# Kernel optimization log

Hardware: AMD Instinct MI355X
Metric: run time of the kernel (lower is better)

## Reference

```python
import jax, jax.numpy as jnp
import numpy as np

N_NODES = 50000
N_EDGES = 640000
IN_CH = 128
OUT_CH = 128
HID = 2 * OUT_CH  # 256


def _glorot(key, shape):
    fan_in, fan_out = shape
    lim = np.sqrt(6.0 / (fan_in + fan_out)).astype(np.float32)
    return jax.random.uniform(key, shape, jnp.float32, -lim, lim)


def setup_inputs() -> dict:
    key = jax.random.key(0)
    ks = jax.random.split(key, 8)
    x = jax.random.normal(ks[0], (N_NODES, IN_CH), jnp.float32)
    edge_index = jax.random.randint(ks[1], (2, N_EDGES), 0, N_NODES, jnp.int64)
    # SAGEConv layer 1: lin_l (neighbor branch, with bias), lin_r (root branch, no bias)
    w1_l = _glorot(ks[2], (IN_CH, HID))
    b1_l = jnp.zeros((HID,), jnp.float32)
    w1_r = _glorot(ks[3], (IN_CH, HID))
    # SAGEConv layer 2
    w2_l = _glorot(ks[4], (HID, OUT_CH))
    b2_l = jnp.zeros((OUT_CH,), jnp.float32)
    w2_r = _glorot(ks[5], (HID, OUT_CH))
    return {"x": x, "edge_index": edge_index,
            "w1_l": w1_l, "b1_l": b1_l, "w1_r": w1_r,
            "w2_l": w2_l, "b2_l": b2_l, "w2_r": w2_r}


def _sage_conv(x, src, dst, w_l, b_l, w_r):
    # mean aggregation of source-node features onto destination nodes
    msgs = x[src]                                       # [E, C] gather
    agg = jax.ops.segment_sum(msgs, dst, num_segments=N_NODES)  # [N, C]
    cnt = jax.ops.segment_sum(jnp.ones((src.shape[0],), x.dtype), dst,
                              num_segments=N_NODES)     # [N]
    mean = agg / jnp.maximum(cnt, 1.0)[:, None]
    # out = lin_l(mean_neighbors) + lin_r(x_root)
    return mean @ w_l + b_l + x @ w_r


def reference(x, edge_index, w1_l, b1_l, w1_r, w2_l, b2_l, w2_r):
    src, dst = edge_index[0], edge_index[1]
    h = _sage_conv(x, src, dst, w1_l, b1_l, w1_r)
    h = jax.nn.relu(h)
    return _sage_conv(h, src, dst, w2_l, b2_l, w2_r)
```

## Files before the change

### kernel.cpp

```cpp
#include <hip/hip_runtime.h>

#define N_NODES 50000
#define N_EDGES 640000
#define IN_CH 128
#define OUT_CH 128
#define HID 256
#define M_PAD 50048
#define CAP 64

typedef unsigned int uint;
typedef unsigned short ushort;

__device__ __forceinline__ ushort f2b(float f) {
    uint u = __float_as_uint(f);
    u += 0x7FFFu + ((u >> 16) & 1u);
    return (ushort)(u >> 16);
}
__device__ __forceinline__ float b2f_lo(uint u) { return __uint_as_float(u << 16); }
__device__ __forceinline__ float b2f_hi(uint u) { return __uint_as_float(u & 0xFFFF0000u); }
__device__ __forceinline__ uint packb(float lo, float hi) {
    return (uint)f2b(lo) | ((uint)f2b(hi) << 16);
}

__device__ __forceinline__ void gload_lds16(const ushort* g, ushort* l) {
    __builtin_amdgcn_global_load_lds(
        (const __attribute__((address_space(1))) void*)g,
        (__attribute__((address_space(3))) void*)l, 16, 0, 0);
}

__global__ __launch_bounds__(256) void prep(
    const int* __restrict__ src, const int* __restrict__ dst,
    const float* __restrict__ x, const float* __restrict__ w1l,
    const float* __restrict__ w1r, const float* __restrict__ w2l,
    const float* __restrict__ w2r, int* __restrict__ cnt,
    int* __restrict__ col, ushort* __restrict__ xcat,
    ushort* __restrict__ w1f, ushort* __restrict__ w2f) {
    int b = blockIdx.x;
    if (b < 2500) {
        int e = b * 256 + threadIdx.x;
        int d = dst[e];
        int p = atomicAdd(&cnt[d], 1);
        if (p < CAP) col[d * CAP + p] = src[e];
    } else {
        int id = (b - 2500) * 256 + threadIdx.x;
        if (id < 800000) {
            long long base = (long long)id * 8;
            float4 a = *(const float4*)(x + base);
            float4 c = *(const float4*)(x + base + 4);
            uint4 o;
            o.x = packb(a.x, a.y);
            o.y = packb(a.z, a.w);
            o.z = packb(c.x, c.y);
            o.w = packb(c.z, c.w);
            int row = id >> 4;
            int cc = id & 15;
            ((uint4*)xcat)[(size_t)row * 32 + 16 + cc] = o;
        } else if (id < 865536) {
            int i = id - 800000;
            int n0 = i >> 12, kk = (i >> 9) & 7, lane = (i >> 3) & 63, j = i & 7;
            int n = n0 * 16 + (lane & 15);
            int k = kk * 32 + (lane >> 4) * 8 + j;
            float v = (k < 128) ? w1l[k * 256 + n] : w1r[(k - 128) * 256 + n];
            w1f[i] = f2b(v);
        } else {
            int i = id - 865536;
            int n0 = i >> 12, kk = (i >> 9) & 7, lane = (i >> 3) & 63, j = i & 7;
            int n = n0 * 16 + (lane & 15);
            int k = kk * 32 + (lane >> 4) * 8 + j;
            float v = (n < 128) ? w2l[k * 128 + n] : w2r[k * 128 + (n - 128)];
            w2f[i] = f2b(v);
        }
    }
}

__global__ __launch_bounds__(256) void aggregate_mean1(
    const int* __restrict__ cnt, const int* __restrict__ col,
    ushort* __restrict__ xcat) {
    int t = blockIdx.x * 256 + threadIdx.x;
    int node = t >> 4;
    int q = t & 15;
    if (node >= N_NODES) return;
    int degf = cnt[node];
    int deg = min(degf, CAP);
    const int* cb = col + node * CAP;
    float acc[8] = {0.f, 0.f, 0.f, 0.f, 0.f, 0.f, 0.f, 0.f};
    const uint4* f4 = (const uint4*)xcat;
    int j = 0;
    for (; j + 4 <= deg; j += 4) {
        int4 s4 = *(const int4*)(cb + j);
        uint4 v0 = f4[(size_t)s4.x * 32 + 16 + q];
        uint4 v1 = f4[(size_t)s4.y * 32 + 16 + q];
        uint4 v2 = f4[(size_t)s4.z * 32 + 16 + q];
        uint4 v3 = f4[(size_t)s4.w * 32 + 16 + q];
        acc[0] += b2f_lo(v0.x) + b2f_lo(v1.x) + b2f_lo(v2.x) + b2f_lo(v3.x);
        acc[1] += b2f_hi(v0.x) + b2f_hi(v1.x) + b2f_hi(v2.x) + b2f_hi(v3.x);
        acc[2] += b2f_lo(v0.y) + b2f_lo(v1.y) + b2f_lo(v2.y) + b2f_lo(v3.y);
        acc[3] += b2f_hi(v0.y) + b2f_hi(v1.y) + b2f_hi(v2.y) + b2f_hi(v3.y);
        acc[4] += b2f_lo(v0.z) + b2f_lo(v1.z) + b2f_lo(v2.z) + b2f_lo(v3.z);
        acc[5] += b2f_hi(v0.z) + b2f_hi(v1.z) + b2f_hi(v2.z) + b2f_hi(v3.z);
        acc[6] += b2f_lo(v0.w) + b2f_lo(v1.w) + b2f_lo(v2.w) + b2f_lo(v3.w);
        acc[7] += b2f_hi(v0.w) + b2f_hi(v1.w) + b2f_hi(v2.w) + b2f_hi(v3.w);
    }
    for (; j < deg; ++j) {
        uint4 v = f4[(size_t)cb[j] * 32 + 16 + q];
        acc[0] += b2f_lo(v.x); acc[1] += b2f_hi(v.x);
        acc[2] += b2f_lo(v.y); acc[3] += b2f_hi(v.y);
        acc[4] += b2f_lo(v.z); acc[5] += b2f_hi(v.z);
        acc[6] += b2f_lo(v.w); acc[7] += b2f_hi(v.w);
    }
    float inv = 1.0f / fmaxf((float)degf, 1.0f);
    uint4 o;
    o.x = packb(acc[0] * inv, acc[1] * inv);
    o.y = packb(acc[2] * inv, acc[3] * inv);
    o.z = packb(acc[4] * inv, acc[5] * inv);
    o.w = packb(acc[6] * inv, acc[7] * inv);
    ((uint4*)xcat)[(size_t)node * 32 + q] = o;
}

__global__ __launch_bounds__(256) void combine2(
    const ushort* __restrict__ hw, const int* __restrict__ cnt,
    const int* __restrict__ col, const float* __restrict__ bias,
    float* __restrict__ out) {
    int t = blockIdx.x * 256 + threadIdx.x;
    int node = t >> 4;
    int q = t & 15;
    if (node >= N_NODES) return;
    int degf = cnt[node];
    int deg = min(degf, CAP);
    const int* cb = col + node * CAP;
    float acc[8] = {0.f, 0.f, 0.f, 0.f, 0.f, 0.f, 0.f, 0.f};
    const uint4* f4 = (const uint4*)hw;
    int j = 0;
    for (; j + 4 <= deg; j += 4) {
        int4 s4 = *(const int4*)(cb + j);
        uint4 v0 = f4[(size_t)s4.x * 32 + q];
        uint4 v1 = f4[(size_t)s4.y * 32 + q];
        uint4 v2 = f4[(size_t)s4.z * 32 + q];
        uint4 v3 = f4[(size_t)s4.w * 32 + q];
        acc[0] += b2f_lo(v0.x) + b2f_lo(v1.x) + b2f_lo(v2.x) + b2f_lo(v3.x);
        acc[1] += b2f_hi(v0.x) + b2f_hi(v1.x) + b2f_hi(v2.x) + b2f_hi(v3.x);
        acc[2] += b2f_lo(v0.y) + b2f_lo(v1.y) + b2f_lo(v2.y) + b2f_lo(v3.y);
        acc[3] += b2f_hi(v0.y) + b2f_hi(v1.y) + b2f_hi(v2.y) + b2f_hi(v3.y);
        acc[4] += b2f_lo(v0.z) + b2f_lo(v1.z) + b2f_lo(v2.z) + b2f_lo(v3.z);
        acc[5] += b2f_hi(v0.z) + b2f_hi(v1.z) + b2f_hi(v2.z) + b2f_hi(v3.z);
        acc[6] += b2f_lo(v0.w) + b2f_lo(v1.w) + b2f_lo(v2.w) + b2f_lo(v3.w);
        acc[7] += b2f_hi(v0.w) + b2f_hi(v1.w) + b2f_hi(v2.w) + b2f_hi(v3.w);
    }
    for (; j < deg; ++j) {
        uint4 v = f4[(size_t)cb[j] * 32 + q];
        acc[0] += b2f_lo(v.x); acc[1] += b2f_hi(v.x);
        acc[2] += b2f_lo(v.y); acc[3] += b2f_hi(v.y);
        acc[4] += b2f_lo(v.z); acc[5] += b2f_hi(v.z);
        acc[6] += b2f_lo(v.w); acc[7] += b2f_hi(v.w);
    }
    float inv = 1.0f / fmaxf((float)degf, 1.0f);
    uint4 r = f4[(size_t)node * 32 + 16 + q];
    float4 b0 = *(const float4*)(bias + q * 8);
    float4 b1 = *(const float4*)(bias + q * 8 + 4);
    float4 o0, o1;
    o0.x = acc[0] * inv + b2f_lo(r.x) + b0.x;
    o0.y = acc[1] * inv + b2f_hi(r.x) + b0.y;
    o0.z = acc[2] * inv + b2f_lo(r.y) + b0.z;
    o0.w = acc[3] * inv + b2f_hi(r.y) + b0.w;
    o1.x = acc[4] * inv + b2f_lo(r.z) + b1.x;
    o1.y = acc[5] * inv + b2f_hi(r.z) + b1.y;
    o1.z = acc[6] * inv + b2f_lo(r.w) + b1.z;
    o1.w = acc[7] * inv + b2f_hi(r.w) + b1.w;
    *(float4*)(out + (size_t)node * 128 + q * 8) = o0;
    *(float4*)(out + (size_t)node * 128 + q * 8 + 4) = o1;
}

using bf16x8 = __attribute__((ext_vector_type(8))) short;
using f32x4  = __attribute__((ext_vector_type(4))) float;

__global__ __launch_bounds__(256) void fused_gemm(
    const ushort* __restrict__ A, const ushort* __restrict__ w1f,
    const ushort* __restrict__ w2f, const float* __restrict__ b1,
    ushort* __restrict__ hw) {
    __shared__ alignas(16) ushort tile[32 * 256];

    const int tid = threadIdx.x;
    const int lane = tid & 63;
    const int wave = tid >> 6;
    const int quad = lane >> 4;
    const int l16 = lane & 15;
    const int bm = blockIdx.x * 32;

#pragma unroll
    for (int r = 0; r < 4; ++r) {
        int row = r * 8 + (tid >> 5);
        int c = tid & 31;
        int src = (c & 24) | ((c & 7) ^ (row & 7));
        gload_lds16(A + (size_t)(bm + row) * 256 + src * 8, &tile[row * 256 + c * 8]);
    }

    f32x4 acc[2][4];
#pragma unroll
    for (int rt = 0; rt < 2; ++rt)
#pragma unroll
        for (int ct = 0; ct < 4; ++ct) acc[rt][ct] = (f32x4){0.f, 0.f, 0.f, 0.f};

    const size_t bstep = 64 * 8;
    const ushort* w1b = w1f + (((size_t)(wave * 4) * 8) * 64 + lane) * 8;
    const ushort* w2b = w2f + (((size_t)(wave * 4) * 8) * 64 + lane) * 8;

    bf16x8 bc[4], bn[4];
#pragma unroll
    for (int ct = 0; ct < 4; ++ct)
        bc[ct] = *(const bf16x8*)(w1b + (size_t)ct * 8 * bstep);

    __syncthreads();

#pragma unroll
    for (int kk = 0; kk < 8; ++kk) {
        if (kk < 7) {
#pragma unroll
            for (int ct = 0; ct < 4; ++ct)
                bn[ct] = *(const bf16x8*)(w1b + ((size_t)ct * 8 + kk + 1) * bstep);
        }
        bf16x8 af[2];
#pragma unroll
        for (int rt = 0; rt < 2; ++rt) {
            int row = rt * 16 + l16;
            int c = kk * 4 + quad;
            int slot = (c & 24) | ((c & 7) ^ (row & 7));
            af[rt] = *(const bf16x8*)&tile[row * 256 + slot * 8];
        }
#pragma unroll
        for (int ct = 0; ct < 4; ++ct) {
#pragma unroll
            for (int rt = 0; rt < 2; ++rt)
                acc[rt][ct] = __builtin_amdgcn_mfma_f32_16x16x32_bf16(
                    af[rt], bc[ct], acc[rt][ct], 0, 0, 0);
        }
#pragma unroll
        for (int ct = 0; ct < 4; ++ct) bc[ct] = bn[ct];
    }
    __syncthreads();

#pragma unroll
    for (int ct = 0; ct < 4; ++ct) {
        int colg = wave * 64 + ct * 16 + l16;
        float bv = b1[colg];
        int cc = colg >> 3;
        int off = colg & 7;
#pragma unroll
        for (int rt = 0; rt < 2; ++rt) {
#pragma unroll
            for (int reg = 0; reg < 4; ++reg) {
                int row = rt * 16 + quad * 4 + reg;
                int slot = (cc & 24) | ((cc & 7) ^ (row & 7));
                tile[row * 256 + slot * 8 + off] = f2b(fmaxf(acc[rt][ct][reg] + bv, 0.0f));
            }
        }
    }

#pragma unroll
    for (int rt = 0; rt < 2; ++rt)
#pragma unroll
        for (int ct = 0; ct < 4; ++ct) acc[rt][ct] = (f32x4){0.f, 0.f, 0.f, 0.f};

#pragma unroll
    for (int ct = 0; ct < 4; ++ct)
        bc[ct] = *(const bf16x8*)(w2b + (size_t)ct * 8 * bstep);

    __syncthreads();

#pragma unroll
    for (int kk = 0; kk < 8; ++kk) {
        if (kk < 7) {
#pragma unroll
            for (int ct = 0; ct < 4; ++ct)
                bn[ct] = *(const bf16x8*)(w2b + ((size_t)ct * 8 + kk + 1) * bstep);
        }
        bf16x8 af[2];
#pragma unroll
        for (int rt = 0; rt < 2; ++rt) {
            int row = rt * 16 + l16;
            int c = kk * 4 + quad;
            int slot = (c & 24) | ((c & 7) ^ (row & 7));
            af[rt] = *(const bf16x8*)&tile[row * 256 + slot * 8];
        }
#pragma unroll
        for (int ct = 0; ct < 4; ++ct) {
#pragma unroll
            for (int rt = 0; rt < 2; ++rt)
                acc[rt][ct] = __builtin_amdgcn_mfma_f32_16x16x32_bf16(
                    af[rt], bc[ct], acc[rt][ct], 0, 0, 0);
        }
#pragma unroll
        for (int ct = 0; ct < 4; ++ct) bc[ct] = bn[ct];
    }
    __syncthreads();

#pragma unroll
    for (int ct = 0; ct < 4; ++ct) {
        int colg = wave * 64 + ct * 16 + l16;
        int cc = colg >> 3;
        int off = colg & 7;
#pragma unroll
        for (int rt = 0; rt < 2; ++rt) {
#pragma unroll
            for (int reg = 0; reg < 4; ++reg) {
                int row = rt * 16 + quad * 4 + reg;
                int slot = (cc & 24) | ((cc & 7) ^ (row & 7));
                tile[row * 256 + slot * 8 + off] = f2b(acc[rt][ct][reg]);
            }
        }
    }
    __syncthreads();
#pragma unroll
    for (int r = 0; r < 4; ++r) {
        int row = r * 8 + (tid >> 5);
        int c = tid & 31;
        int slot = (c & 24) | ((c & 7) ^ (row & 7));
        uint4 v = *(const uint4*)&tile[row * 256 + slot * 8];
        *(uint4*)(hw + (size_t)(bm + row) * 256 + c * 8) = v;
    }
}

extern "C" void kernel_launch(void* const* d_in, const int* in_sizes, int n_in,
                              void* d_out, int out_size, void* d_ws, size_t ws_size,
                              hipStream_t stream) {
    const float* x    = (const float*)d_in[0];
    const int*   ei   = (const int*)d_in[1];
    const float* w1_l = (const float*)d_in[2];
    const float* b1_l = (const float*)d_in[3];
    const float* w1_r = (const float*)d_in[4];
    const float* w2_l = (const float*)d_in[5];
    const float* b2_l = (const float*)d_in[6];
    const float* w2_r = (const float*)d_in[7];
    float* out = (float*)d_out;

    const int* src = ei;
    const int* dst = ei + N_EDGES;

    int* cnt = (int*)d_ws;
    int* col = cnt + N_NODES;
    size_t int_bytes = (size_t)(N_NODES + N_NODES * CAP) * 4;
    size_t ofs = (int_bytes + 15) & ~(size_t)15;
    ushort* xcat = (ushort*)((char*)d_ws + ofs);
    ushort* hw   = xcat + (size_t)M_PAD * HID;
    ushort* w1f  = hw + (size_t)M_PAD * HID;
    ushort* w2f  = w1f + HID * HID;

    hipMemsetAsync(cnt, 0, (size_t)N_NODES * sizeof(int), stream);

    prep<<<6137, 256, 0, stream>>>(src, dst, x, w1_l, w1_r, w2_l, w2_r,
                                   cnt, col, xcat, w1f, w2f);

    aggregate_mean1<<<N_NODES * 16 / 256, 256, 0, stream>>>(cnt, col, xcat);
    fused_gemm<<<M_PAD / 32, 256, 0, stream>>>(xcat, w1f, w2f, b1_l, hw);
    combine2<<<N_NODES * 16 / 256, 256, 0, stream>>>(hw, cnt, col, b2_l, out);
}
```

Measured before the change: 230.2 us.

## Fuse layer-1 mean aggregation into the fused GEMM kernel's LDS tile load

Removes the separate aggregate_mean1 kernel. Each fused_gemm block now gathers and averages neighbor features for its 32 rows and writes the bf16 mean straight into a swizzled LDS tile, while the root half is loaded asynchronously. The shared tile is split into left and right halves. This saves one launch and the global write and re-read of the aggregated half of xcat. In exchange, the GEMM blocks now stall on irregular gathers before their MFMA work, and each thread handles 16 channels with only 2-edge unrolling, so there is less memory-level parallelism than before.

Measured after the change: 226.7 us, median of 2. About the same (-1.5%).

```diff
diff --git a/kernel.cpp b/kernel.cpp
--- a/kernel.cpp
+++ b/kernel.cpp
@@ -73,50 +73,6 @@
     }
 }
 
-__global__ __launch_bounds__(256) void aggregate_mean1(
-    const int* __restrict__ cnt, const int* __restrict__ col,
-    ushort* __restrict__ xcat) {
-    int t = blockIdx.x * 256 + threadIdx.x;
-    int node = t >> 4;
-    int q = t & 15;
-    if (node >= N_NODES) return;
-    int degf = cnt[node];
-    int deg = min(degf, CAP);
-    const int* cb = col + node * CAP;
-    float acc[8] = {0.f, 0.f, 0.f, 0.f, 0.f, 0.f, 0.f, 0.f};
-    const uint4* f4 = (const uint4*)xcat;
-    int j = 0;
-    for (; j + 4 <= deg; j += 4) {
-        int4 s4 = *(const int4*)(cb + j);
-        uint4 v0 = f4[(size_t)s4.x * 32 + 16 + q];
-        uint4 v1 = f4[(size_t)s4.y * 32 + 16 + q];
-        uint4 v2 = f4[(size_t)s4.z * 32 + 16 + q];
-        uint4 v3 = f4[(size_t)s4.w * 32 + 16 + q];
-        acc[0] += b2f_lo(v0.x) + b2f_lo(v1.x) + b2f_lo(v2.x) + b2f_lo(v3.x);
-        acc[1] += b2f_hi(v0.x) + b2f_hi(v1.x) + b2f_hi(v2.x) + b2f_hi(v3.x);
-        acc[2] += b2f_lo(v0.y) + b2f_lo(v1.y) + b2f_lo(v2.y) + b2f_lo(v3.y);
-        acc[3] += b2f_hi(v0.y) + b2f_hi(v1.y) + b2f_hi(v2.y) + b2f_hi(v3.y);
-        acc[4] += b2f_lo(v0.z) + b2f_lo(v1.z) + b2f_lo(v2.z) + b2f_lo(v3.z);
-        acc[5] += b2f_hi(v0.z) + b2f_hi(v1.z) + b2f_hi(v2.z) + b2f_hi(v3.z);
-        acc[6] += b2f_lo(v0.w) + b2f_lo(v1.w) + b2f_lo(v2.w) + b2f_lo(v3.w);
-        acc[7] += b2f_hi(v0.w) + b2f_hi(v1.w) + b2f_hi(v2.w) + b2f_hi(v3.w);
-    }
-    for (; j < deg; ++j) {
-        uint4 v = f4[(size_t)cb[j] * 32 + 16 + q];
-        acc[0] += b2f_lo(v.x); acc[1] += b2f_hi(v.x);
-        acc[2] += b2f_lo(v.y); acc[3] += b2f_hi(v.y);
-        acc[4] += b2f_lo(v.z); acc[5] += b2f_hi(v.z);
-        acc[6] += b2f_lo(v.w); acc[7] += b2f_hi(v.w);
-    }
-    float inv = 1.0f / fmaxf((float)degf, 1.0f);
-    uint4 o;
-    o.x = packb(acc[0] * inv, acc[1] * inv);
-    o.y = packb(acc[2] * inv, acc[3] * inv);
-    o.z = packb(acc[4] * inv, acc[5] * inv);
-    o.w = packb(acc[6] * inv, acc[7] * inv);
-    ((uint4*)xcat)[(size_t)node * 32 + q] = o;
-}
-
 __global__ __launch_bounds__(256) void combine2(
     const ushort* __restrict__ hw, const int* __restrict__ cnt,
     const int* __restrict__ col, const float* __restrict__ bias,
@@ -174,10 +130,12 @@
 using f32x4  = __attribute__((ext_vector_type(4))) float;
 
 __global__ __launch_bounds__(256) void fused_gemm(
-    const ushort* __restrict__ A, const ushort* __restrict__ w1f,
+    const ushort* __restrict__ A, const int* __restrict__ cnt,
+    const int* __restrict__ col, const ushort* __restrict__ w1f,
     const ushort* __restrict__ w2f, const float* __restrict__ b1,
     ushort* __restrict__ hw) {
-    __shared__ alignas(16) ushort tile[32 * 256];
+    __shared__ alignas(16) ushort tileL[32 * 128];
+    __shared__ alignas(16) ushort tileR[32 * 128];
 
     const int tid = threadIdx.x;
     const int lane = tid & 63;
@@ -187,27 +145,92 @@
     const int bm = blockIdx.x * 32;
 
 #pragma unroll
-    for (int r = 0; r < 4; ++r) {
-        int row = r * 8 + (tid >> 5);
-        int c = tid & 31;
-        int src = (c & 24) | ((c & 7) ^ (row & 7));
-        gload_lds16(A + (size_t)(bm + row) * 256 + src * 8, &tile[row * 256 + c * 8]);
-    }
-
-    f32x4 acc[2][4];
-#pragma unroll
-    for (int rt = 0; rt < 2; ++rt)
-#pragma unroll
-        for (int ct = 0; ct < 4; ++ct) acc[rt][ct] = (f32x4){0.f, 0.f, 0.f, 0.f};
+    for (int r = 0; r < 2; ++r) {
+        int row = r * 16 + (tid >> 4);
+        int kc = tid & 15;
+        int src = 16 + ((kc & 8) | ((kc & 7) ^ (row & 7)));
+        gload_lds16(A + (size_t)(bm + row) * 256 + src * 8,
+                    &tileR[row * 128 + kc * 8]);
+    }
 
     const size_t bstep = 64 * 8;
     const ushort* w1b = w1f + (((size_t)(wave * 4) * 8) * 64 + lane) * 8;
     const ushort* w2b = w2f + (((size_t)(wave * 4) * 8) * 64 + lane) * 8;
-
     bf16x8 bc[4], bn[4];
 #pragma unroll
     for (int ct = 0; ct < 4; ++ct)
         bc[ct] = *(const bf16x8*)(w1b + (size_t)ct * 8 * bstep);
+
+    {
+        int rw = tid >> 3;
+        int q8 = tid & 7;
+        int node = bm + rw;
+        int degf = 0, deg = 0;
+        if (node < N_NODES) { degf = cnt[node]; deg = min(degf, CAP); }
+        const int* cb = col + (size_t)node * CAP;
+        const uint4* f4 = (const uint4*)A;
+        float acc[16];
+#pragma unroll
+        for (int i = 0; i < 16; ++i) acc[i] = 0.f;
+        int j = 0;
+        for (; j + 2 <= deg; j += 2) {
+            int2 s2 = *(const int2*)(cb + j);
+            uint4 a0 = f4[(size_t)s2.x * 32 + 16 + q8 * 2];
+            uint4 a1 = f4[(size_t)s2.x * 32 + 17 + q8 * 2];
+            uint4 c0 = f4[(size_t)s2.y * 32 + 16 + q8 * 2];
+            uint4 c1 = f4[(size_t)s2.y * 32 + 17 + q8 * 2];
+            acc[0] += b2f_lo(a0.x) + b2f_lo(c0.x);
+            acc[1] += b2f_hi(a0.x) + b2f_hi(c0.x);
+            acc[2] += b2f_lo(a0.y) + b2f_lo(c0.y);
+            acc[3] += b2f_hi(a0.y) + b2f_hi(c0.y);
+            acc[4] += b2f_lo(a0.z) + b2f_lo(c0.z);
+            acc[5] += b2f_hi(a0.z) + b2f_hi(c0.z);
+            acc[6] += b2f_lo(a0.w) + b2f_lo(c0.w);
+            acc[7] += b2f_hi(a0.w) + b2f_hi(c0.w);
+            acc[8]  += b2f_lo(a1.x) + b2f_lo(c1.x);
+            acc[9]  += b2f_hi(a1.x) + b2f_hi(c1.x);
+            acc[10] += b2f_lo(a1.y) + b2f_lo(c1.y);
+            acc[11] += b2f_hi(a1.y) + b2f_hi(c1.y);
+            acc[12] += b2f_lo(a1.z) + b2f_lo(c1.z);
+            acc[13] += b2f_hi(a1.z) + b2f_hi(c1.z);
+            acc[14] += b2f_lo(a1.w) + b2f_lo(c1.w);
+            acc[15] += b2f_hi(a1.w) + b2f_hi(c1.w);
+        }
+        if (j < deg) {
+            int s = cb[j];
+            uint4 a0 = f4[(size_t)s * 32 + 16 + q8 * 2];
+            uint4 a1 = f4[(size_t)s * 32 + 17 + q8 * 2];
+            acc[0] += b2f_lo(a0.x);  acc[1] += b2f_hi(a0.x);
+            acc[2] += b2f_lo(a0.y);  acc[3] += b2f_hi(a0.y);
+            acc[4] += b2f_lo(a0.z);  acc[5] += b2f_hi(a0.z);
+            acc[6] += b2f_lo(a0.w);  acc[7] += b2f_hi(a0.w);
+            acc[8]  += b2f_lo(a1.x); acc[9]  += b2f_hi(a1.x);
+            acc[10] += b2f_lo(a1.y); acc[11] += b2f_hi(a1.y);
+            acc[12] += b2f_lo(a1.z); acc[13] += b2f_hi(a1.z);
+            acc[14] += b2f_lo(a1.w); acc[15] += b2f_hi(a1.w);
+        }
+        float inv = 1.0f / fmaxf((float)degf, 1.0f);
+        int kc0 = q8 * 2, kc1 = q8 * 2 + 1;
+        int s0 = (kc0 & 8) | ((kc0 & 7) ^ (rw & 7));
+        int s1 = (kc1 & 8) | ((kc1 & 7) ^ (rw & 7));
+        uint4 o0, o1;
+        o0.x = packb(acc[0] * inv, acc[1] * inv);
+        o0.y = packb(acc[2] * inv, acc[3] * inv);
+        o0.z = packb(acc[4] * inv, acc[5] * inv);
+        o0.w = packb(acc[6] * inv, acc[7] * inv);
+        o1.x = packb(acc[8] * inv, acc[9] * inv);
+        o1.y = packb(acc[10] * inv, acc[11] * inv);
+        o1.z = packb(acc[12] * inv, acc[13] * inv);
+        o1.w = packb(acc[14] * inv, acc[15] * inv);
+        *(uint4*)&tileL[rw * 128 + s0 * 8] = o0;
+        *(uint4*)&tileL[rw * 128 + s1 * 8] = o1;
+    }
+
+    f32x4 acc[2][4];
+#pragma unroll
+    for (int rt = 0; rt < 2; ++rt)
+#pragma unroll
+        for (int ct = 0; ct < 4; ++ct) acc[rt][ct] = (f32x4){0.f, 0.f, 0.f, 0.f};
 
     __syncthreads();
 
@@ -223,8 +246,10 @@
         for (int rt = 0; rt < 2; ++rt) {
             int row = rt * 16 + l16;
             int c = kk * 4 + quad;
-            int slot = (c & 24) | ((c & 7) ^ (row & 7));
-            af[rt] = *(const bf16x8*)&tile[row * 256 + slot * 8];
+            int hc = c & 15;
+            int slot = (hc & 8) | ((hc & 7) ^ (row & 7));
+            const ushort* base = (c < 16) ? tileL : tileR;
+            af[rt] = *(const bf16x8*)&base[row * 128 + slot * 8];
         }
 #pragma unroll
         for (int ct = 0; ct < 4; ++ct) {
@@ -243,14 +268,16 @@
         int colg = wave * 64 + ct * 16 + l16;
         float bv = b1[colg];
         int cc = colg >> 3;
+        int hc = cc & 15;
         int off = colg & 7;
+        ushort* base = (cc < 16) ? tileL : tileR;
 #pragma unroll
         for (int rt = 0; rt < 2; ++rt) {
 #pragma unroll
             for (int reg = 0; reg < 4; ++reg) {
                 int row = rt * 16 + quad * 4 + reg;
-                int slot = (cc & 24) | ((cc & 7) ^ (row & 7));
-                tile[row * 256 + slot * 8 + off] = f2b(fmaxf(acc[rt][ct][reg] + bv, 0.0f));
+                int slot = (hc & 8) | ((hc & 7) ^ (row & 7));
+                base[row * 128 + slot * 8 + off] = f2b(fmaxf(acc[rt][ct][reg] + bv, 0.0f));
             }
         }
     }
@@ -278,8 +305,10 @@
         for (int rt = 0; rt < 2; ++rt) {
             int row = rt * 16 + l16;
             int c = kk * 4 + quad;
-            int slot = (c & 24) | ((c & 7) ^ (row & 7));
-            af[rt] = *(const bf16x8*)&tile[row * 256 + slot * 8];
+            int hc = c & 15;
+            int slot = (hc & 8) | ((hc & 7) ^ (row & 7));
+            const ushort* base = (c < 16) ? tileL : tileR;
+            af[rt] = *(const bf16x8*)&base[row * 128 + slot * 8];
         }
 #pragma unroll
         for (int ct = 0; ct < 4; ++ct) {
@@ -297,14 +326,16 @@
     for (int ct = 0; ct < 4; ++ct) {
         int colg = wave * 64 + ct * 16 + l16;
         int cc = colg >> 3;
+        int hc = cc & 15;
         int off = colg & 7;
+        ushort* base = (cc < 16) ? tileL : tileR;
 #pragma unroll
         for (int rt = 0; rt < 2; ++rt) {
 #pragma unroll
             for (int reg = 0; reg < 4; ++reg) {
                 int row = rt * 16 + quad * 4 + reg;
-                int slot = (cc & 24) | ((cc & 7) ^ (row & 7));
-                tile[row * 256 + slot * 8 + off] = f2b(acc[rt][ct][reg]);
+                int slot = (hc & 8) | ((hc & 7) ^ (row & 7));
+                base[row * 128 + slot * 8 + off] = f2b(acc[rt][ct][reg]);
             }
         }
     }
@@ -313,8 +344,10 @@
     for (int r = 0; r < 4; ++r) {
         int row = r * 8 + (tid >> 5);
         int c = tid & 31;
-        int slot = (c & 24) | ((c & 7) ^ (row & 7));
-        uint4 v = *(const uint4*)&tile[row * 256 + slot * 8];
+        int hc = c & 15;
+        int slot = (hc & 8) | ((hc & 7) ^ (row & 7));
+        const ushort* base = (c < 16) ? tileL : tileR;
+        uint4 v = *(const uint4*)&base[row * 128 + slot * 8];
         *(uint4*)(hw + (size_t)(bm + row) * 256 + c * 8) = v;
     }
 }
@@ -346,10 +379,9 @@
 
     hipMemsetAsync(cnt, 0, (size_t)N_NODES * sizeof(int), stream);
 
-    prep<<<6137, 256, 0, stream>>>(src, dst, x, w1_l, w1_r, w2_l, w2_r,
-                                   cnt, col, xcat, w1f, w2f);
-
-    aggregate_mean1<<<N_NODES * 16 / 256, 256, 0, stream>>>(cnt, col, xcat);
-    fused_gemm<<<M_PAD / 32, 256, 0, stream>>>(xcat, w1f, w2f, b1_l, hw);
+    prep<<<2500 + 3637, 256, 0, stream>>>(src, dst, x, w1_l, w1_r, w2_l, w2_r,
+                                          cnt, col, xcat, w1f, w2f);
+
+    fused_gemm<<<M_PAD / 32, 256, 0, stream>>>(xcat, cnt, col, w1f, w2f, b1_l, hw);
     combine2<<<N_NODES * 16 / 256, 256, 0, stream>>>(hw, cnt, col, b2_l, out);
 }
```

## Split gather tables into channel slices for cache-friendly neighbor aggregation

Applied to the files above, without the earlier changes.

Stores the bf16 node features and the GEMM output in a sliced layout, where each 16-channel slice is contiguous across all nodes. Aggregation and combine kernels now assign each block one slice and 128 nodes, so concurrently running blocks gather from a much smaller working set that fits in L2/LLC. This costs an extra write of x in the slice layout during prep and more scattered row stores from the GEMM epilogue, and each gather is now only 32 bytes per node per slice instead of one full row.

Result: slower. 243.1 us (+5.6%).

```diff
diff --git a/kernel.cpp b/kernel.cpp
--- a/kernel.cpp
+++ b/kernel.cpp
@@ -34,7 +34,8 @@
     const float* __restrict__ w1r, const float* __restrict__ w2l,
     const float* __restrict__ w2r, int* __restrict__ cnt,
     int* __restrict__ col, ushort* __restrict__ xcat,
-    ushort* __restrict__ w1f, ushort* __restrict__ w2f) {
+    ushort* __restrict__ xs, ushort* __restrict__ w1f,
+    ushort* __restrict__ w2f) {
     int b = blockIdx.x;
     if (b < 2500) {
         int e = b * 256 + threadIdx.x;
@@ -55,6 +56,7 @@
             int row = id >> 4;
             int cc = id & 15;
             ((uint4*)xcat)[(size_t)row * 32 + 16 + cc] = o;
+            ((uint4*)xs)[(size_t)((cc >> 1) * M_PAD + row) * 2 + (cc & 1)] = o;
         } else if (id < 865536) {
             int i = id - 800000;
             int n0 = i >> 12, kk = (i >> 9) & 7, lane = (i >> 3) & 63, j = i & 7;
@@ -73,25 +75,27 @@
     }
 }
 
-__global__ __launch_bounds__(256) void aggregate_mean1(
+__global__ __launch_bounds__(256) void aggregate_s(
     const int* __restrict__ cnt, const int* __restrict__ col,
-    ushort* __restrict__ xcat) {
-    int t = blockIdx.x * 256 + threadIdx.x;
-    int node = t >> 4;
-    int q = t & 15;
+    const ushort* __restrict__ xs, ushort* __restrict__ xcat) {
+    int slice = blockIdx.x & 7;
+    int chunk = blockIdx.x >> 3;
+    int node = chunk * 128 + (threadIdx.x >> 1);
+    int half = threadIdx.x & 1;
     if (node >= N_NODES) return;
     int degf = cnt[node];
     int deg = min(degf, CAP);
-    const int* cb = col + node * CAP;
+    const int* cb = col + (size_t)node * CAP;
+    const uint4* xv = (const uint4*)xs;
+    const size_t gb = (size_t)slice * M_PAD * 2 + half;
     float acc[8] = {0.f, 0.f, 0.f, 0.f, 0.f, 0.f, 0.f, 0.f};
-    const uint4* f4 = (const uint4*)xcat;
     int j = 0;
     for (; j + 4 <= deg; j += 4) {
         int4 s4 = *(const int4*)(cb + j);
-        uint4 v0 = f4[(size_t)s4.x * 32 + 16 + q];
-        uint4 v1 = f4[(size_t)s4.y * 32 + 16 + q];
-        uint4 v2 = f4[(size_t)s4.z * 32 + 16 + q];
-        uint4 v3 = f4[(size_t)s4.w * 32 + 16 + q];
+        uint4 v0 = xv[gb + (size_t)s4.x * 2];
+        uint4 v1 = xv[gb + (size_t)s4.y * 2];
+        uint4 v2 = xv[gb + (size_t)s4.z * 2];
+        uint4 v3 = xv[gb + (size_t)s4.w * 2];
         acc[0] += b2f_lo(v0.x) + b2f_lo(v1.x) + b2f_lo(v2.x) + b2f_lo(v3.x);
         acc[1] += b2f_hi(v0.x) + b2f_hi(v1.x) + b2f_hi(v2.x) + b2f_hi(v3.x);
         acc[2] += b2f_lo(v0.y) + b2f_lo(v1.y) + b2f_lo(v2.y) + b2f_lo(v3.y);
@@ -102,7 +106,7 @@
         acc[7] += b2f_hi(v0.w) + b2f_hi(v1.w) + b2f_hi(v2.w) + b2f_hi(v3.w);
     }
     for (; j < deg; ++j) {
-        uint4 v = f4[(size_t)cb[j] * 32 + 16 + q];
+        uint4 v = xv[gb + (size_t)cb[j] * 2];
         acc[0] += b2f_lo(v.x); acc[1] += b2f_hi(v.x);
         acc[2] += b2f_lo(v.y); acc[3] += b2f_hi(v.y);
         acc[4] += b2f_lo(v.z); acc[5] += b2f_hi(v.z);
@@ -114,29 +118,31 @@
     o.y = packb(acc[2] * inv, acc[3] * inv);
     o.z = packb(acc[4] * inv, acc[5] * inv);
     o.w = packb(acc[6] * inv, acc[7] * inv);
-    ((uint4*)xcat)[(size_t)node * 32 + q] = o;
-}
-
-__global__ __launch_bounds__(256) void combine2(
-    const ushort* __restrict__ hw, const int* __restrict__ cnt,
+    ((uint4*)xcat)[(size_t)node * 32 + slice * 2 + half] = o;
+}
+
+__global__ __launch_bounds__(256) void combine2_s(
+    const ushort* __restrict__ hws, const int* __restrict__ cnt,
     const int* __restrict__ col, const float* __restrict__ bias,
     float* __restrict__ out) {
-    int t = blockIdx.x * 256 + threadIdx.x;
-    int node = t >> 4;
-    int q = t & 15;
+    int slice = blockIdx.x & 7;
+    int chunk = blockIdx.x >> 3;
+    int node = chunk * 128 + (threadIdx.x >> 1);
+    int half = threadIdx.x & 1;
     if (node >= N_NODES) return;
     int degf = cnt[node];
     int deg = min(degf, CAP);
-    const int* cb = col + node * CAP;
+    const int* cb = col + (size_t)node * CAP;
+    const uint4* hv = (const uint4*)hws;
+    const size_t gb = (size_t)slice * M_PAD * 2 + half;
     float acc[8] = {0.f, 0.f, 0.f, 0.f, 0.f, 0.f, 0.f, 0.f};
-    const uint4* f4 = (const uint4*)hw;
     int j = 0;
     for (; j + 4 <= deg; j += 4) {
         int4 s4 = *(const int4*)(cb + j);
-        uint4 v0 = f4[(size_t)s4.x * 32 + q];
-        uint4 v1 = f4[(size_t)s4.y * 32 + q];
-        uint4 v2 = f4[(size_t)s4.z * 32 + q];
-        uint4 v3 = f4[(size_t)s4.w * 32 + q];
+        uint4 v0 = hv[gb + (size_t)s4.x * 2];
+        uint4 v1 = hv[gb + (size_t)s4.y * 2];
+        uint4 v2 = hv[gb + (size_t)s4.z * 2];
+        uint4 v3 = hv[gb + (size_t)s4.w * 2];
         acc[0] += b2f_lo(v0.x) + b2f_lo(v1.x) + b2f_lo(v2.x) + b2f_lo(v3.x);
         acc[1] += b2f_hi(v0.x) + b2f_hi(v1.x) + b2f_hi(v2.x) + b2f_hi(v3.x);
         acc[2] += b2f_lo(v0.y) + b2f_lo(v1.y) + b2f_lo(v2.y) + b2f_lo(v3.y);
@@ -147,16 +153,17 @@
         acc[7] += b2f_hi(v0.w) + b2f_hi(v1.w) + b2f_hi(v2.w) + b2f_hi(v3.w);
     }
     for (; j < deg; ++j) {
-        uint4 v = f4[(size_t)cb[j] * 32 + q];
+        uint4 v = hv[gb + (size_t)cb[j] * 2];
         acc[0] += b2f_lo(v.x); acc[1] += b2f_hi(v.x);
         acc[2] += b2f_lo(v.y); acc[3] += b2f_hi(v.y);
         acc[4] += b2f_lo(v.z); acc[5] += b2f_hi(v.z);
         acc[6] += b2f_lo(v.w); acc[7] += b2f_hi(v.w);
     }
     float inv = 1.0f / fmaxf((float)degf, 1.0f);
-    uint4 r = f4[(size_t)node * 32 + 16 + q];
-    float4 b0 = *(const float4*)(bias + q * 8);
-    float4 b1 = *(const float4*)(bias + q * 8 + 4);
+    uint4 r = hv[(size_t)((8 + slice) * M_PAD + node) * 2 + half];
+    int c0 = slice * 16 + half * 8;
+    float4 b0 = *(const float4*)(bias + c0);
+    float4 b1 = *(const float4*)(bias + c0 + 4);
     float4 o0, o1;
     o0.x = acc[0] * inv + b2f_lo(r.x) + b0.x;
     o0.y = acc[1] * inv + b2f_hi(r.x) + b0.y;
@@ -166,8 +173,8 @@
     o1.y = acc[5] * inv + b2f_hi(r.z) + b1.y;
     o1.z = acc[6] * inv + b2f_lo(r.w) + b1.z;
     o1.w = acc[7] * inv + b2f_hi(r.w) + b1.w;
-    *(float4*)(out + (size_t)node * 128 + q * 8) = o0;
-    *(float4*)(out + (size_t)node * 128 + q * 8 + 4) = o1;
+    *(float4*)(out + (size_t)node * 128 + c0) = o0;
+    *(float4*)(out + (size_t)node * 128 + c0 + 4) = o1;
 }
 
 using bf16x8 = __attribute__((ext_vector_type(8))) short;
@@ -176,7 +183,7 @@
 __global__ __launch_bounds__(256) void fused_gemm(
     const ushort* __restrict__ A, const ushort* __restrict__ w1f,
     const ushort* __restrict__ w2f, const float* __restrict__ b1,
-    ushort* __restrict__ hw) {
+    ushort* __restrict__ hws) {
     __shared__ alignas(16) ushort tile[32 * 256];
 
     const int tid = threadIdx.x;
@@ -310,12 +317,14 @@
     }
     __syncthreads();
 #pragma unroll
-    for (int r = 0; r < 4; ++r) {
-        int row = r * 8 + (tid >> 5);
-        int c = tid & 31;
-        int slot = (c & 24) | ((c & 7) ^ (row & 7));
-        uint4 v = *(const uint4*)&tile[row * 256 + slot * 8];
-        *(uint4*)(hw + (size_t)(bm + row) * 256 + c * 8) = v;
+    for (int it = 0; it < 4; ++it) {
+        int sidx = it * 4 + wave;
+        int node = lane >> 1;
+        int hf = lane & 1;
+        int c = sidx * 2 + hf;
+        int slot = (c & 24) | ((c & 7) ^ (node & 7));
+        uint4 v = *(const uint4*)&tile[node * 256 + slot * 8];
+        ((uint4*)hws)[(size_t)(sidx * M_PAD + bm + node) * 2 + hf] = v;
     }
 }
 
@@ -340,16 +349,17 @@
     size_t int_bytes = (size_t)(N_NODES + N_NODES * CAP) * 4;
     size_t ofs = (int_bytes + 15) & ~(size_t)15;
     ushort* xcat = (ushort*)((char*)d_ws + ofs);
-    ushort* hw   = xcat + (size_t)M_PAD * HID;
-    ushort* w1f  = hw + (size_t)M_PAD * HID;
+    ushort* xs   = xcat + (size_t)M_PAD * HID;
+    ushort* hws  = xs + (size_t)8 * M_PAD * 16;
+    ushort* w1f  = hws + (size_t)16 * M_PAD * 16;
     ushort* w2f  = w1f + HID * HID;
 
     hipMemsetAsync(cnt, 0, (size_t)N_NODES * sizeof(int), stream);
 
-    prep<<<6137, 256, 0, stream>>>(src, dst, x, w1_l, w1_r, w2_l, w2_r,
-                                   cnt, col, xcat, w1f, w2f);
-
-    aggregate_mean1<<<N_NODES * 16 / 256, 256, 0, stream>>>(cnt, col, xcat);
-    fused_gemm<<<M_PAD / 32, 256, 0, stream>>>(xcat, w1f, w2f, b1_l, hw);
-    combine2<<<N_NODES * 16 / 256, 256, 0, stream>>>(hw, cnt, col, b2_l, out);
-}
+    prep<<<2500 + 3637, 256, 0, stream>>>(src, dst, x, w1_l, w1_r, w2_l, w2_r,
+                                          cnt, col, xcat, xs, w1f, w2f);
+
+    aggregate_s<<<8 * 391, 256, 0, stream>>>(cnt, col, xs, xcat);
+    fused_gemm<<<M_PAD / 32, 256, 0, stream>>>(xcat, w1f, w2f, b1_l, hws);
+    combine2_s<<<8 * 391, 256, 0, stream>>>(hws, cnt, col, b2_l, out);
+}
```

## Two-level bucketed CSR build and persistent double-buffered fused GEMM

Applied to the files above, without the earlier changes.

The edge-to-CSR construction changes from per-node global atomics to a two-stage scheme. Edges are first appended as (dst,src) pairs into 196 coarse bins of 256 nodes each, using padded bin counters. A new binplace kernel then scatters each bin into the per-node col lists using shared-memory atomics, which is meant to cut global atomic contention and the scattered writes. The fused GEMM becomes a persistent kernel with 512 blocks that loops over row tiles and prefetches the next A tile into a second LDS buffer while computing the current one. The costs are an extra kernel launch, an intermediate bin buffer, a hard BIN_CAP per bin, doubled LDS use and extra barriers per tile.

New measurement: 246.1 us. 6.9% more time.

```diff
diff --git a/kernel.cpp b/kernel.cpp
--- a/kernel.cpp
+++ b/kernel.cpp
@@ -7,6 +7,9 @@
 #define HID 256
 #define M_PAD 50048
 #define CAP 64
+#define BINS 196
+#define BIN_CAP 4096
+#define GEMM_GRID 512
 
 typedef unsigned int uint;
 typedef unsigned short ushort;
@@ -32,15 +35,17 @@
     const int* __restrict__ src, const int* __restrict__ dst,
     const float* __restrict__ x, const float* __restrict__ w1l,
     const float* __restrict__ w1r, const float* __restrict__ w2l,
-    const float* __restrict__ w2r, int* __restrict__ cnt,
-    int* __restrict__ col, ushort* __restrict__ xcat,
+    const float* __restrict__ w2r, int* __restrict__ bcnt,
+    int2* __restrict__ bins, ushort* __restrict__ xcat,
     ushort* __restrict__ w1f, ushort* __restrict__ w2f) {
     int b = blockIdx.x;
     if (b < 2500) {
         int e = b * 256 + threadIdx.x;
         int d = dst[e];
-        int p = atomicAdd(&cnt[d], 1);
-        if (p < CAP) col[d * CAP + p] = src[e];
+        int s = src[e];
+        int bb = d >> 8;
+        int p = atomicAdd(&bcnt[bb * 32], 1);
+        if (p < BIN_CAP) bins[(size_t)bb * BIN_CAP + p] = make_int2(d, s);
     } else {
         int id = (b - 2500) * 256 + threadIdx.x;
         if (id < 800000) {
@@ -73,6 +78,26 @@
     }
 }
 
+__global__ __launch_bounds__(256) void binplace(
+    const int* __restrict__ bcnt, const int2* __restrict__ bins,
+    int* __restrict__ cnt, int* __restrict__ col) {
+    __shared__ int lcnt[256];
+    int b = blockIdx.x;
+    lcnt[threadIdx.x] = 0;
+    __syncthreads();
+    int n = min(bcnt[b * 32], BIN_CAP);
+    int base = b << 8;
+    const int2* bb = bins + (size_t)b * BIN_CAP;
+    for (int i = threadIdx.x; i < n; i += 256) {
+        int2 e = bb[i];
+        int p = atomicAdd(&lcnt[e.x - base], 1);
+        if (p < CAP) col[(size_t)e.x * CAP + p] = e.y;
+    }
+    __syncthreads();
+    int node = base + threadIdx.x;
+    if (node < N_NODES) cnt[node] = lcnt[threadIdx.x];
+}
+
 __global__ __launch_bounds__(256) void aggregate_mean1(
     const int* __restrict__ cnt, const int* __restrict__ col,
     ushort* __restrict__ xcat) {
@@ -177,145 +202,169 @@
     const ushort* __restrict__ A, const ushort* __restrict__ w1f,
     const ushort* __restrict__ w2f, const float* __restrict__ b1,
     ushort* __restrict__ hw) {
-    __shared__ alignas(16) ushort tile[32 * 256];
+    __shared__ alignas(16) ushort buf[2][32 * 256];
 
     const int tid = threadIdx.x;
     const int lane = tid & 63;
     const int wave = tid >> 6;
     const int quad = lane >> 4;
     const int l16 = lane & 15;
-    const int bm = blockIdx.x * 32;
-
-#pragma unroll
-    for (int r = 0; r < 4; ++r) {
-        int row = r * 8 + (tid >> 5);
-        int c = tid & 31;
-        int src = (c & 24) | ((c & 7) ^ (row & 7));
-        gload_lds16(A + (size_t)(bm + row) * 256 + src * 8, &tile[row * 256 + c * 8]);
-    }
-
-    f32x4 acc[2][4];
-#pragma unroll
-    for (int rt = 0; rt < 2; ++rt)
-#pragma unroll
-        for (int ct = 0; ct < 4; ++ct) acc[rt][ct] = (f32x4){0.f, 0.f, 0.f, 0.f};
+    const int srow = tid >> 5;
+    const int sc = tid & 31;
+    const int NT = M_PAD / 32;
 
     const size_t bstep = 64 * 8;
     const ushort* w1b = w1f + (((size_t)(wave * 4) * 8) * 64 + lane) * 8;
     const ushort* w2b = w2f + (((size_t)(wave * 4) * 8) * 64 + lane) * 8;
 
-    bf16x8 bc[4], bn[4];
-#pragma unroll
-    for (int ct = 0; ct < 4; ++ct)
-        bc[ct] = *(const bf16x8*)(w1b + (size_t)ct * 8 * bstep);
-
+    {
+        int t = blockIdx.x;
+#pragma unroll
+        for (int r = 0; r < 4; ++r) {
+            int row = r * 8 + srow;
+            int sl = (sc & 24) | ((sc & 7) ^ (row & 7));
+            gload_lds16(A + (size_t)(t * 32 + row) * 256 + sl * 8,
+                        &buf[0][row * 256 + sc * 8]);
+        }
+    }
+    int cur = 0;
     __syncthreads();
 
-#pragma unroll
-    for (int kk = 0; kk < 8; ++kk) {
-        if (kk < 7) {
-#pragma unroll
-            for (int ct = 0; ct < 4; ++ct)
-                bn[ct] = *(const bf16x8*)(w1b + ((size_t)ct * 8 + kk + 1) * bstep);
-        }
-        bf16x8 af[2];
-#pragma unroll
-        for (int rt = 0; rt < 2; ++rt) {
-            int row = rt * 16 + l16;
-            int c = kk * 4 + quad;
-            int slot = (c & 24) | ((c & 7) ^ (row & 7));
-            af[rt] = *(const bf16x8*)&tile[row * 256 + slot * 8];
-        }
+    for (int t = blockIdx.x; t < NT; t += GEMM_GRID) {
+        ushort* tile = buf[cur];
+        const int bm = t * 32;
+
+        int tn = t + GEMM_GRID;
+        if (tn < NT) {
+            ushort* nb = buf[cur ^ 1];
+#pragma unroll
+            for (int r = 0; r < 4; ++r) {
+                int row = r * 8 + srow;
+                int sl = (sc & 24) | ((sc & 7) ^ (row & 7));
+                gload_lds16(A + (size_t)(tn * 32 + row) * 256 + sl * 8,
+                            &nb[row * 256 + sc * 8]);
+            }
+        }
+
+        f32x4 acc[2][4];
+#pragma unroll
+        for (int rt = 0; rt < 2; ++rt)
+#pragma unroll
+            for (int ct = 0; ct < 4; ++ct) acc[rt][ct] = (f32x4){0.f, 0.f, 0.f, 0.f};
+
+        bf16x8 bc[4], bn[4];
+#pragma unroll
+        for (int ct = 0; ct < 4; ++ct)
+            bc[ct] = *(const bf16x8*)(w1b + (size_t)ct * 8 * bstep);
+
+#pragma unroll
+        for (int kk = 0; kk < 8; ++kk) {
+            if (kk < 7) {
+#pragma unroll
+                for (int ct = 0; ct < 4; ++ct)
+                    bn[ct] = *(const bf16x8*)(w1b + ((size_t)ct * 8 + kk + 1) * bstep);
+            }
+            bf16x8 af[2];
+#pragma unroll
+            for (int rt = 0; rt < 2; ++rt) {
+                int row = rt * 16 + l16;
+                int c = kk * 4 + quad;
+                int slot = (c & 24) | ((c & 7) ^ (row & 7));
+                af[rt] = *(const bf16x8*)&tile[row * 256 + slot * 8];
+            }
+#pragma unroll
+            for (int ct = 0; ct < 4; ++ct) {
+#pragma unroll
+                for (int rt = 0; rt < 2; ++rt)
+                    acc[rt][ct] = __builtin_amdgcn_mfma_f32_16x16x32_bf16(
+                        af[rt], bc[ct], acc[rt][ct], 0, 0, 0);
+            }
+#pragma unroll
+            for (int ct = 0; ct < 4; ++ct) bc[ct] = bn[ct];
+        }
+        __syncthreads();
+
 #pragma unroll
         for (int ct = 0; ct < 4; ++ct) {
-#pragma unroll
-            for (int rt = 0; rt < 2; ++rt)
-                acc[rt][ct] = __builtin_amdgcn_mfma_f32_16x16x32_bf16(
-                    af[rt], bc[ct], acc[rt][ct], 0, 0, 0);
-        }
-#pragma unroll
-        for (int ct = 0; ct < 4; ++ct) bc[ct] = bn[ct];
-    }
-    __syncthreads();
-
-#pragma unroll
-    for (int ct = 0; ct < 4; ++ct) {
-        int colg = wave * 64 + ct * 16 + l16;
-        float bv = b1[colg];
-        int cc = colg >> 3;
-        int off = colg & 7;
-#pragma unroll
-        for (int rt = 0; rt < 2; ++rt) {
-#pragma unroll
-            for (int reg = 0; reg < 4; ++reg) {
-                int row = rt * 16 + quad * 4 + reg;
-                int slot = (cc & 24) | ((cc & 7) ^ (row & 7));
-                tile[row * 256 + slot * 8 + off] = f2b(fmaxf(acc[rt][ct][reg] + bv, 0.0f));
-            }
-        }
-    }
-
-#pragma unroll
-    for (int rt = 0; rt < 2; ++rt)
-#pragma unroll
-        for (int ct = 0; ct < 4; ++ct) acc[rt][ct] = (f32x4){0.f, 0.f, 0.f, 0.f};
-
-#pragma unroll
-    for (int ct = 0; ct < 4; ++ct)
-        bc[ct] = *(const bf16x8*)(w2b + (size_t)ct * 8 * bstep);
-
-    __syncthreads();
-
-#pragma unroll
-    for (int kk = 0; kk < 8; ++kk) {
-        if (kk < 7) {
-#pragma unroll
-            for (int ct = 0; ct < 4; ++ct)
-                bn[ct] = *(const bf16x8*)(w2b + ((size_t)ct * 8 + kk + 1) * bstep);
-        }
-        bf16x8 af[2];
-#pragma unroll
-        for (int rt = 0; rt < 2; ++rt) {
-            int row = rt * 16 + l16;
-            int c = kk * 4 + quad;
-            int slot = (c & 24) | ((c & 7) ^ (row & 7));
-            af[rt] = *(const bf16x8*)&tile[row * 256 + slot * 8];
-        }
+            int colg = wave * 64 + ct * 16 + l16;
+            float bv = b1[colg];
+            int cc = colg >> 3;
+            int off = colg & 7;
+#pragma unroll
+            for (int rt = 0; rt < 2; ++rt) {
+#pragma unroll
+                for (int reg = 0; reg < 4; ++reg) {
+                    int row = rt * 16 + quad * 4 + reg;
+                    int slot = (cc & 24) | ((cc & 7) ^ (row & 7));
+                    tile[row * 256 + slot * 8 + off] =
+                        f2b(fmaxf(acc[rt][ct][reg] + bv, 0.0f));
+                }
+            }
+        }
+
+#pragma unroll
+        for (int rt = 0; rt < 2; ++rt)
+#pragma unroll
+            for (int ct = 0; ct < 4; ++ct) acc[rt][ct] = (f32x4){0.f, 0.f, 0.f, 0.f};
+
+#pragma unroll
+        for (int ct = 0; ct < 4; ++ct)
+            bc[ct] = *(const bf16x8*)(w2b + (size_t)ct * 8 * bstep);
+
+        __syncthreads();
+
+#pragma unroll
+        for (int kk = 0; kk < 8; ++kk) {
+            if (kk < 7) {
+#pragma unroll
+                for (int ct = 0; ct < 4; ++ct)
+                    bn[ct] = *(const bf16x8*)(w2b + ((size_t)ct * 8 + kk + 1) * bstep);
+            }
+            bf16x8 af[2];
+#pragma unroll
+            for (int rt = 0; rt < 2; ++rt) {
+                int row = rt * 16 + l16;
+                int c = kk * 4 + quad;
+                int slot = (c & 24) | ((c & 7) ^ (row & 7));
+                af[rt] = *(const bf16x8*)&tile[row * 256 + slot * 8];
+            }
+#pragma unroll
+            for (int ct = 0; ct < 4; ++ct) {
+#pragma unroll
+                for (int rt = 0; rt < 2; ++rt)
+                    acc[rt][ct] = __builtin_amdgcn_mfma_f32_16x16x32_bf16(
+                        af[rt], bc[ct], acc[rt][ct], 0, 0, 0);
+            }
+#pragma unroll
+            for (int ct = 0; ct < 4; ++ct) bc[ct] = bn[ct];
+        }
+        __syncthreads();
+
 #pragma unroll
         for (int ct = 0; ct < 4; ++ct) {
-#pragma unroll
-            for (int rt = 0; rt < 2; ++rt)
-                acc[rt][ct] = __builtin_amdgcn_mfma_f32_16x16x32_bf16(
-                    af[rt], bc[ct], acc[rt][ct], 0, 0, 0);
-        }
-#pragma unroll
-        for (int ct = 0; ct < 4; ++ct) bc[ct] = bn[ct];
-    }
-    __syncthreads();
-
-#pragma unroll
-    for (int ct = 0; ct < 4; ++ct) {
-        int colg = wave * 64 + ct * 16 + l16;
-        int cc = colg >> 3;
-        int off = colg & 7;
-#pragma unroll
-        for (int rt = 0; rt < 2; ++rt) {
-#pragma unroll
-            for (int reg = 0; reg < 4; ++reg) {
-                int row = rt * 16 + quad * 4 + reg;
-                int slot = (cc & 24) | ((cc & 7) ^ (row & 7));
-                tile[row * 256 + slot * 8 + off] = f2b(acc[rt][ct][reg]);
-            }
-        }
-    }
-    __syncthreads();
-#pragma unroll
-    for (int r = 0; r < 4; ++r) {
-        int row = r * 8 + (tid >> 5);
-        int c = tid & 31;
-        int slot = (c & 24) | ((c & 7) ^ (row & 7));
-        uint4 v = *(const uint4*)&tile[row * 256 + slot * 8];
-        *(uint4*)(hw + (size_t)(bm + row) * 256 + c * 8) = v;
+            int colg = wave * 64 + ct * 16 + l16;
+            int cc = colg >> 3;
+            int off = colg & 7;
+#pragma unroll
+            for (int rt = 0; rt < 2; ++rt) {
+#pragma unroll
+                for (int reg = 0; reg < 4; ++reg) {
+                    int row = rt * 16 + quad * 4 + reg;
+                    int slot = (cc & 24) | ((cc & 7) ^ (row & 7));
+                    tile[row * 256 + slot * 8 + off] = f2b(acc[rt][ct][reg]);
+                }
+            }
+        }
+        __syncthreads();
+#pragma unroll
+        for (int r = 0; r < 4; ++r) {
+            int row = r * 8 + srow;
+            int slot = (sc & 24) | ((sc & 7) ^ (row & 7));
+            uint4 v = *(const uint4*)&tile[row * 256 + slot * 8];
+            *(uint4*)(hw + (size_t)(bm + row) * 256 + sc * 8) = v;
+        }
+        __syncthreads();
+        cur ^= 1;
     }
 }
 
@@ -337,19 +386,25 @@
 
     int* cnt = (int*)d_ws;
     int* col = cnt + N_NODES;
-    size_t int_bytes = (size_t)(N_NODES + N_NODES * CAP) * 4;
-    size_t ofs = (int_bytes + 15) & ~(size_t)15;
+    int* bcnt = col + (size_t)N_NODES * CAP;
+    int2* bins = (int2*)(bcnt + BINS * 32);
+    size_t int_bytes = (size_t)(N_NODES + N_NODES * CAP + BINS * 32) * 4
+                       + (size_t)BINS * BIN_CAP * 8;
+    size_t ofs = ((size_t)((char*)bins - (char*)d_ws) + (size_t)BINS * BIN_CAP * 8 + 15)
+                 & ~(size_t)15;
+    (void)int_bytes;
     ushort* xcat = (ushort*)((char*)d_ws + ofs);
     ushort* hw   = xcat + (size_t)M_PAD * HID;
     ushort* w1f  = hw + (size_t)M_PAD * HID;
     ushort* w2f  = w1f + HID * HID;
 
-    hipMemsetAsync(cnt, 0, (size_t)N_NODES * sizeof(int), stream);
-
-    prep<<<6137, 256, 0, stream>>>(src, dst, x, w1_l, w1_r, w2_l, w2_r,
-                                   cnt, col, xcat, w1f, w2f);
+    hipMemsetAsync(bcnt, 0, (size_t)BINS * 32 * sizeof(int), stream);
+
+    prep<<<2500 + 3637, 256, 0, stream>>>(src, dst, x, w1_l, w1_r, w2_l, w2_r,
+                                          bcnt, bins, xcat, w1f, w2f);
+    binplace<<<BINS, 256, 0, stream>>>(bcnt, bins, cnt, col);
 
     aggregate_mean1<<<N_NODES * 16 / 256, 256, 0, stream>>>(cnt, col, xcat);
-    fused_gemm<<<M_PAD / 32, 256, 0, stream>>>(xcat, w1f, w2f, b1_l, hw);
+    fused_gemm<<<GEMM_GRID, 256, 0, stream>>>(xcat, w1f, w2f, b1_l, hw);
     combine2<<<N_NODES * 16 / 256, 256, 0, stream>>>(hw, cnt, col, b2_l, out);
 }
```
